# Kernel tuning notes

Measured on AMD Instinct MI355X. Metric: run time of the kernel, lower is better.

## Reference

```python
import jax, jax.numpy as jnp
import numpy as np

B, T, H, L, O = 128, 1024, 512, 2, 1
SCALE = 0.02  # keep tanh/sigmoid in sane range


def setup_inputs() -> dict:
    key = jax.random.key(0)
    ks = jax.random.split(key, 13)
    return {
        "input": jax.random.normal(ks[0], (B, 8), jnp.float32),
        "hidden": jax.random.normal(ks[1], (L, B, H), jnp.float32) * 0.5,
        "encoder_outputs": jax.random.normal(ks[2], (B, T, H), jnp.float32),
        "attn_w": jax.random.normal(ks[3], (1, (L + 1) * H), jnp.float32) * SCALE,
        "attn_b": jnp.zeros((1,), jnp.float32),
        "comb_w": jax.random.normal(ks[4], (H, H + O), jnp.float32) * SCALE,
        "comb_b": jnp.zeros((H,), jnp.float32),
        "gru_w_ih": jax.random.normal(ks[5], (L, 3 * H, H), jnp.float32) * SCALE,
        "gru_w_hh": jax.random.normal(ks[6], (L, 3 * H, H), jnp.float32) * SCALE,
        "gru_b_ih": jnp.zeros((L, 3 * H), jnp.float32),
        "gru_b_hh": jnp.zeros((L, 3 * H), jnp.float32),
        "out_w": jax.random.normal(ks[7], (O, H), jnp.float32) * SCALE,
        "out_b": jnp.zeros((O,), jnp.float32),
    }


def reference(input, hidden, encoder_outputs, attn_w, attn_b, comb_w, comb_b,
              gru_w_ih, gru_w_hh, gru_b_ih, gru_b_hh, out_w, out_b):
    # input0 = input[:, -1].unsqueeze(1) -> [B, 1]
    input0 = input[:, -1:]
    # hidden [L,B,H] -> hidden_attn [B, L*H]
    hidden_attn = jnp.transpose(hidden, (1, 0, 2)).reshape(hidden.shape[1], -1)
    # Vectorized additive-attention scores (original loops over T):
    # score[b,t] = [hidden_attn_b ; enc_bt] @ attn_w.T + attn_b
    w = attn_w[0]                      # [(L+1)*H]
    w_h, w_e = w[: L * H], w[L * H:]   # [L*H], [H]
    score = (hidden_attn @ w_h)[:, None] + jnp.einsum('bth,h->bt', encoder_outputs, w_e) + attn_b[0]
    attn_weights = jax.nn.softmax(score, axis=1)          # [B, T]
    attn_applied = jnp.einsum('bt,bth->bh', attn_weights, encoder_outputs)  # [B, H]
    # attn_combine + relu (dropout_p = 0 -> identity)
    comb_in = jnp.concatenate([input0, attn_applied], axis=1)  # [B, 1+H]
    x = jax.nn.relu(comb_in @ comb_w.T + comb_b)               # [B, H]
    # single-step multi-layer GRU (PyTorch gate order: r, z, n)
    new_hidden = []
    for l in range(L):
        gx = x @ gru_w_ih[l].T + gru_b_ih[l]             # [B, 3H]
        gh = hidden[l] @ gru_w_hh[l].T + gru_b_hh[l]     # [B, 3H]
        xr, xz, xn = jnp.split(gx, 3, axis=1)
        hr, hz, hn = jnp.split(gh, 3, axis=1)
        r = jax.nn.sigmoid(xr + hr)
        z = jax.nn.sigmoid(xz + hz)
        n = jnp.tanh(xn + r * hn)
        h_new = (1.0 - z) * n + z * hidden[l]
        new_hidden.append(h_new)
        x = h_new
    hidden_out = jnp.stack(new_hidden, axis=0)           # [L, B, H]
    output = x @ out_w.T + out_b                         # [B, O]
    return output, hidden_out, attn_weights[:, None, :]
```

## Files before the change

kernel.cpp:

```cpp
#include <hip/hip_runtime.h>
#include <math.h>

#define B 128
#define T 1024
#define H 512
#define L 2
#define G3H 1536
#define C 8
#define TC 128
#define TT 8
#define NT (TC / TT)
#define KS 4

#define GLOBAL_AS __attribute__((address_space(1)))
#define LDS_AS    __attribute__((address_space(3)))

__global__ __launch_bounds__(256, 4)
void attn_fused_kernel(const float* __restrict__ enc,
                       const float* __restrict__ attn_w,
                       float* __restrict__ score_out,
                       float* __restrict__ part,
                       float* __restrict__ stats) {
    int c = blockIdx.x, b = blockIdx.y;
    int tid = threadIdx.x, lane = tid & 63, wave = tid >> 6;
    __shared__ float tile[2][TT * H];
    __shared__ float s_tile[TT];

    const float4 we0 = *(const float4*)(attn_w + L * H + lane * 8);
    const float4 we1 = *(const float4*)(attn_w + L * H + lane * 8 + 4);

    const float* encb = enc + ((size_t)b * T + c * TC) * H;
    const GLOBAL_AS float* gsrc = (const GLOBAL_AS float*)encb;
    LDS_AS float* ldst = (LDS_AS float*)(&tile[0][0]);

#define STAGE(buf, t0)                                                        \
    {                                                                         \
        const GLOBAL_AS float* g = gsrc + (size_t)(t0) * H;                   \
        LDS_AS float* lb = ldst + (buf) * (TT * H);                           \
        _Pragma("unroll")                                                     \
        for (int k = 0; k < 4; k++) {                                         \
            __builtin_amdgcn_global_load_lds(                                 \
                (const GLOBAL_AS void*)(g + k * 1024 + tid * 4),              \
                (LDS_AS void*)(lb + k * 1024 + tid * 4), 16, 0, 0);           \
        }                                                                     \
    }

    float m_run = -1e30f, l_run = 0.0f;
    float accx = 0.0f, accy = 0.0f;

    STAGE(0, 0);
    for (int t = 0; t < NT; t++) {
        __syncthreads();
        if (t + 1 < NT) STAGE((t + 1) & 1, (t + 1) * TT);
        const float* tb = &tile[t & 1][0];

#pragma unroll
        for (int r = 0; r < 2; r++) {
            int row = wave * 2 + r;
            const float* tr = tb + row * H + lane * 8;
            float4 e0 = *(const float4*)(tr);
            float4 e1 = *(const float4*)(tr + 4);
            float d = e0.x * we0.x + e0.y * we0.y + e0.z * we0.z + e0.w * we0.w
                    + e1.x * we1.x + e1.y * we1.y + e1.z * we1.z + e1.w * we1.w;
#pragma unroll
            for (int off = 32; off; off >>= 1) d += __shfl_xor(d, off);
            if (lane == 0) {
                s_tile[row] = d;
                score_out[b * T + c * TC + t * TT + row] = d;
            }
        }
        __builtin_amdgcn_s_waitcnt(0xC07F);
        __builtin_amdgcn_s_barrier();

        float sarr[TT], tmax = -1e30f;
#pragma unroll
        for (int i = 0; i < TT; i++) {
            sarr[i] = s_tile[i];
            tmax = fmaxf(tmax, sarr[i]);
        }
        float m_new = fmaxf(m_run, tmax);
        float alpha = __expf(m_run - m_new);
        accx *= alpha; accy *= alpha;
        float wsum = 0.0f;
#pragma unroll
        for (int i = 0; i < TT; i++) {
            float w = __expf(sarr[i] - m_new);
            wsum += w;
            accx += w * tb[i * H + tid];
            accy += w * tb[i * H + tid + 256];
        }
        l_run = l_run * alpha + wsum;
        m_run = m_new;
    }
    part[((size_t)c * B + b) * H + tid]       = accx;
    part[((size_t)c * B + b) * H + tid + 256] = accy;
    if (tid == 0) {
        stats[(c * B + b) * 2]     = m_run;
        stats[(c * B + b) * 2 + 1] = l_run;
    }
#undef STAGE
}

__global__ void attn_reduce_kernel(const float* __restrict__ part,
                                   const float* __restrict__ stats,
                                   const float* __restrict__ score,
                                   float* __restrict__ attn_applied,
                                   float* __restrict__ attnw) {
    int b = blockIdx.x, tid = threadIdx.x;
    float mc[C], lc[C], m_fin = -1e30f;
#pragma unroll
    for (int k = 0; k < C; k++) {
        mc[k] = stats[(k * B + b) * 2];
        lc[k] = stats[(k * B + b) * 2 + 1];
        m_fin = fmaxf(m_fin, mc[k]);
    }
    float l_fin = 0.0f;
#pragma unroll
    for (int k = 0; k < C; k++) l_fin += lc[k] * __expf(mc[k] - m_fin);
    float inv = 1.0f / l_fin;
    float ax = 0.0f, ay = 0.0f;
#pragma unroll
    for (int k = 0; k < C; k++) {
        float sc = __expf(mc[k] - m_fin);
        ax += sc * part[((size_t)k * B + b) * H + tid];
        ay += sc * part[((size_t)k * B + b) * H + tid + 256];
    }
    attn_applied[(size_t)b * H + tid]       = ax * inv;
    attn_applied[(size_t)b * H + tid + 256] = ay * inv;
    float4 sv = *(const float4*)(score + b * T + tid * 4);
    float4 ov = { __expf(sv.x - m_fin) * inv, __expf(sv.y - m_fin) * inv,
                  __expf(sv.z - m_fin) * inv, __expf(sv.w - m_fin) * inv };
    *(float4*)(attnw + b * T + tid * 4) = ov;
}

__global__ void comb_kernel(const float* __restrict__ attn_applied,
                            const float* __restrict__ input,
                            const float* __restrict__ comb_w,
                            const float* __restrict__ comb_b,
                            float* __restrict__ x_out) {
    int q = blockIdx.x, b = blockIdx.y, tid = threadIdx.x;
    int lane = tid & 63, wave = tid >> 6;
    float in0 = input[b * 8 + 7];
    float areg[8];
#pragma unroll
    for (int j = 0; j < 8; j++) areg[j] = attn_applied[(size_t)b * H + j * 64 + lane];
    for (int r = 0; r < 32; r++) {
        int h = q * 128 + wave * 32 + r;
        const float* wr = comb_w + (size_t)h * (H + 1);
        float d = 0.0f;
#pragma unroll
        for (int j = 0; j < 8; j++) d += areg[j] * wr[1 + j * 64 + lane];
#pragma unroll
        for (int off = 32; off; off >>= 1) d += __shfl_xor(d, off);
        if (lane == 0)
            x_out[(size_t)b * H + h] = fmaxf(0.0f, d + in0 * wr[0] + comb_b[h]);
    }
}

__global__ void gemm_kernel(const float* __restrict__ A0,
                            const float* __restrict__ A1,
                            const float* __restrict__ W0,
                            const float* __restrict__ W1,
                            float* __restrict__ C0,
                            float* __restrict__ C1) {
    int z = blockIdx.z;
    int sel = z & 1, ks = z >> 1;
    const float* A = sel ? A1 : A0;
    const float* W = sel ? W1 : W0;
    float* Cp = (sel ? C1 : C0) + (size_t)ks * B * G3H;
    __shared__ float As[32][33];
    __shared__ float Ws[32][33];
    int n0 = blockIdx.x * 32, m0 = blockIdx.y * 32;
    int tid = threadIdx.x;
    int lrow = tid >> 3;
    int lcol = (tid & 7) * 4;
    int tm = (tid >> 4) * 2;
    int tn = (tid & 15) * 2;
    float a00 = 0, a01 = 0, a10 = 0, a11 = 0;
    int kbeg = ks * (H / KS), kend = kbeg + H / KS;
    for (int k0 = kbeg; k0 < kend; k0 += 32) {
        float4 av = *(const float4*)(A + (size_t)(m0 + lrow) * H + k0 + lcol);
        float4 wv = *(const float4*)(W + (size_t)(n0 + lrow) * H + k0 + lcol);
        __syncthreads();
        As[lrow][lcol] = av.x; As[lrow][lcol + 1] = av.y;
        As[lrow][lcol + 2] = av.z; As[lrow][lcol + 3] = av.w;
        Ws[lrow][lcol] = wv.x; Ws[lrow][lcol + 1] = wv.y;
        Ws[lrow][lcol + 2] = wv.z; Ws[lrow][lcol + 3] = wv.w;
        __syncthreads();
#pragma unroll
        for (int k = 0; k < 32; k++) {
            float x0 = As[tm][k], x1 = As[tm + 1][k];
            float w0 = Ws[tn][k], w1 = Ws[tn + 1][k];
            a00 += x0 * w0; a01 += x0 * w1;
            a10 += x1 * w0; a11 += x1 * w1;
        }
    }
    Cp[(size_t)(m0 + tm) * G3H + n0 + tn]         = a00;
    Cp[(size_t)(m0 + tm) * G3H + n0 + tn + 1]     = a01;
    Cp[(size_t)(m0 + tm + 1) * G3H + n0 + tn]     = a10;
    Cp[(size_t)(m0 + tm + 1) * G3H + n0 + tn + 1] = a11;
}

__global__ void gates_kernel(const float* __restrict__ gx,
                             const float* __restrict__ gh,
                             const float* __restrict__ b_ih,
                             const float* __restrict__ b_hh,
                             const float* __restrict__ hprev,
                             float* __restrict__ hid_out,
                             float* __restrict__ x_out) {
    int idx = blockIdx.x * 256 + threadIdx.x;
    int b = idx >> 9, h = idx & 511;
    size_t gb = (size_t)b * G3H;
    float xr = b_ih[h], xz = b_ih[H + h], xn = b_ih[2 * H + h];
    float hr = b_hh[h], hz = b_hh[H + h], hn = b_hh[2 * H + h];
#pragma unroll
    for (int k = 0; k < KS; k++) {
        size_t o = (size_t)k * B * G3H + gb;
        xr += gx[o + h];         xz += gx[o + H + h];     xn += gx[o + 2 * H + h];
        hr += gh[o + h];         hz += gh[o + H + h];     hn += gh[o + 2 * H + h];
    }
    float hp = hprev[(size_t)b * H + h];
    float r = 1.0f / (1.0f + expf(-(xr + hr)));
    float z = 1.0f / (1.0f + expf(-(xz + hz)));
    float n = tanhf(xn + r * hn);
    float hnew = (1.0f - z) * n + z * hp;
    hid_out[(size_t)b * H + h] = hnew;
    x_out[(size_t)b * H + h] = hnew;
}

__global__ void out_kernel(const float* __restrict__ x,
                           const float* __restrict__ out_w,
                           const float* __restrict__ out_b,
                           float* __restrict__ out) {
    int b = blockIdx.x, lane = threadIdx.x;
    const float4 w0 = *(const float4*)(out_w + lane * 8);
    const float4 w1 = *(const float4*)(out_w + lane * 8 + 4);
    const float4 x0 = *(const float4*)(x + (size_t)b * H + lane * 8);
    const float4 x1 = *(const float4*)(x + (size_t)b * H + lane * 8 + 4);
    float d = x0.x * w0.x + x0.y * w0.y + x0.z * w0.z + x0.w * w0.w
            + x1.x * w1.x + x1.y * w1.y + x1.z * w1.z + x1.w * w1.w;
#pragma unroll
    for (int off = 32; off; off >>= 1) d += __shfl_xor(d, off);
    if (lane == 0) out[b] = d + out_b[0];
}

extern "C" void kernel_launch(void* const* d_in, const int* in_sizes, int n_in,
                              void* d_out, int out_size, void* d_ws, size_t ws_size,
                              hipStream_t stream) {
    const float* input  = (const float*)d_in[0];
    const float* hidden = (const float*)d_in[1];
    const float* enc    = (const float*)d_in[2];
    const float* attn_w = (const float*)d_in[3];
    const float* comb_w = (const float*)d_in[5];
    const float* comb_b = (const float*)d_in[6];
    const float* w_ih   = (const float*)d_in[7];
    const float* w_hh   = (const float*)d_in[8];
    const float* b_ih   = (const float*)d_in[9];
    const float* b_hh   = (const float*)d_in[10];
    const float* out_w  = (const float*)d_in[11];
    const float* out_b  = (const float*)d_in[12];

    float* out = (float*)d_out;
    float* hid_out = out + B;
    float* attnw   = out + B + L * B * H;

    float* ws      = (float*)d_ws;
    float* score   = ws;
    float* part    = score + B * T;
    float* stats   = part + C * B * H;
    float* attnapp = stats + C * B * 2;
    float* x       = attnapp + B * H;
    float* gx      = x + B * H;
    float* gh      = gx + KS * B * G3H;

    attn_fused_kernel<<<dim3(C, B), 256, 0, stream>>>(enc, attn_w, score, part, stats);
    attn_reduce_kernel<<<dim3(B), 256, 0, stream>>>(part, stats, score, attnapp, attnw);
    comb_kernel<<<dim3(4, B), 256, 0, stream>>>(attnapp, input, comb_w, comb_b, x);

    for (int l = 0; l < L; l++) {
        const float* hl = hidden + (size_t)l * B * H;
        gemm_kernel<<<dim3(G3H / 32, B / 32, 2 * KS), 256, 0, stream>>>(
            x, hl,
            w_ih + (size_t)l * G3H * H, w_hh + (size_t)l * G3H * H,
            gx, gh);
        gates_kernel<<<dim3(B * H / 256), 256, 0, stream>>>(
            gx, gh, b_ih + l * G3H, b_hh + l * G3H, hl,
            hid_out + (size_t)l * B * H, x);
    }
    out_kernel<<<dim3(B), 64, 0, stream>>>(x, out_w, out_b, out);
}
```

Baseline: 459.5 us.

## Replace fp32 tiled GRU GEMM with bf16 MFMA matrix-core kernel

The shared-memory fp32 GEMM for the GRU gate projections is replaced by a single-wavefront kernel that converts fp32 operands to bf16 in registers and issues 16x16x32 bf16 MFMA instructions, computing a 64x16 output tile per wave. The K-split factor is also halved, which reduces the partial-sum traffic the gates kernel has to read back. The intent is to move this matmul onto the matrix cores and drop the LDS staging and barriers. In exchange, operands are rounded to bf16, which lowers precision, and each 64-thread block loads its fragments straight from global memory with no reuse through LDS.

Result: faster. 445.4 us (-3.1%).

```diff
diff --git a/kernel.cpp b/kernel.cpp
--- a/kernel.cpp
+++ b/kernel.cpp
@@ -10,10 +10,13 @@
 #define TC 128
 #define TT 8
 #define NT (TC / TT)
-#define KS 4
+#define KS 2
 
 #define GLOBAL_AS __attribute__((address_space(1)))
 #define LDS_AS    __attribute__((address_space(3)))
+
+typedef __attribute__((ext_vector_type(8))) short bf16x8;
+typedef __attribute__((ext_vector_type(4))) float f32x4;
 
 __global__ __launch_bounds__(256, 4)
 void attn_fused_kernel(const float* __restrict__ enc,
@@ -157,48 +160,61 @@
     }
 }
 
-__global__ void gemm_kernel(const float* __restrict__ A0,
-                            const float* __restrict__ A1,
-                            const float* __restrict__ W0,
-                            const float* __restrict__ W1,
-                            float* __restrict__ C0,
-                            float* __restrict__ C1) {
-    int z = blockIdx.z;
-    int sel = z & 1, ks = z >> 1;
+__device__ inline short f2bf(float f) {
+    union { float f; unsigned u; } v; v.f = f;
+    unsigned r = v.u + 0x7fffu + ((v.u >> 16) & 1u);
+    return (short)(r >> 16);
+}
+
+__device__ inline bf16x8 load_frag(const float* __restrict__ p) {
+    float4 a = *(const float4*)p;
+    float4 b = *(const float4*)(p + 4);
+    bf16x8 r;
+    r[0] = f2bf(a.x); r[1] = f2bf(a.y); r[2] = f2bf(a.z); r[3] = f2bf(a.w);
+    r[4] = f2bf(b.x); r[5] = f2bf(b.y); r[6] = f2bf(b.z); r[7] = f2bf(b.w);
+    return r;
+}
+
+__global__ __launch_bounds__(64)
+void gemm_mfma_kernel(const float* __restrict__ A0,
+                      const float* __restrict__ A1,
+                      const float* __restrict__ W0,
+                      const float* __restrict__ W1,
+                      float* __restrict__ C0,
+                      float* __restrict__ C1) {
+    int job = blockIdx.x;
+    int sel = job & 1, ks = (job >> 1) & (KS - 1), mh = (job >> 2) & 1, nt = job >> 3;
     const float* A = sel ? A1 : A0;
     const float* W = sel ? W1 : W0;
     float* Cp = (sel ? C1 : C0) + (size_t)ks * B * G3H;
-    __shared__ float As[32][33];
-    __shared__ float Ws[32][33];
-    int n0 = blockIdx.x * 32, m0 = blockIdx.y * 32;
-    int tid = threadIdx.x;
-    int lrow = tid >> 3;
-    int lcol = (tid & 7) * 4;
-    int tm = (tid >> 4) * 2;
-    int tn = (tid & 15) * 2;
-    float a00 = 0, a01 = 0, a10 = 0, a11 = 0;
-    int kbeg = ks * (H / KS), kend = kbeg + H / KS;
-    for (int k0 = kbeg; k0 < kend; k0 += 32) {
-        float4 av = *(const float4*)(A + (size_t)(m0 + lrow) * H + k0 + lcol);
-        float4 wv = *(const float4*)(W + (size_t)(n0 + lrow) * H + k0 + lcol);
-        __syncthreads();
-        As[lrow][lcol] = av.x; As[lrow][lcol + 1] = av.y;
-        As[lrow][lcol + 2] = av.z; As[lrow][lcol + 3] = av.w;
-        Ws[lrow][lcol] = wv.x; Ws[lrow][lcol + 1] = wv.y;
-        Ws[lrow][lcol + 2] = wv.z; Ws[lrow][lcol + 3] = wv.w;
-        __syncthreads();
-#pragma unroll
-        for (int k = 0; k < 32; k++) {
-            float x0 = As[tm][k], x1 = As[tm + 1][k];
-            float w0 = Ws[tn][k], w1 = Ws[tn + 1][k];
-            a00 += x0 * w0; a01 += x0 * w1;
-            a10 += x1 * w0; a11 += x1 * w1;
-        }
-    }
-    Cp[(size_t)(m0 + tm) * G3H + n0 + tn]         = a00;
-    Cp[(size_t)(m0 + tm) * G3H + n0 + tn + 1]     = a01;
-    Cp[(size_t)(m0 + tm + 1) * G3H + n0 + tn]     = a10;
-    Cp[(size_t)(m0 + tm + 1) * G3H + n0 + tn + 1] = a11;
+    int lane = threadIdx.x;
+    int row16 = lane & 15, quad = lane >> 4;
+    int n0 = nt * 16, m0 = mh * 64;
+    int kb = ks * (H / KS);
+    const float* Wp = W + (size_t)(n0 + row16) * H + kb + quad * 8;
+    const float* Ap = A + (size_t)(m0 + row16) * H + kb + quad * 8;
+    f32x4 acc0 = {0.f, 0.f, 0.f, 0.f}, acc1 = acc0, acc2 = acc0, acc3 = acc0;
+#pragma unroll 2
+    for (int k = 0; k < H / KS; k += 32) {
+        bf16x8 bw = load_frag(Wp + k);
+        bf16x8 a0 = load_frag(Ap + k);
+        bf16x8 a1 = load_frag(Ap + 16 * H + k);
+        bf16x8 a2 = load_frag(Ap + 32 * H + k);
+        bf16x8 a3 = load_frag(Ap + 48 * H + k);
+        acc0 = __builtin_amdgcn_mfma_f32_16x16x32_bf16(a0, bw, acc0, 0, 0, 0);
+        acc1 = __builtin_amdgcn_mfma_f32_16x16x32_bf16(a1, bw, acc1, 0, 0, 0);
+        acc2 = __builtin_amdgcn_mfma_f32_16x16x32_bf16(a2, bw, acc2, 0, 0, 0);
+        acc3 = __builtin_amdgcn_mfma_f32_16x16x32_bf16(a3, bw, acc3, 0, 0, 0);
+    }
+    int col = n0 + row16;
+    int rb = m0 + quad * 4;
+#pragma unroll
+    for (int reg = 0; reg < 4; reg++) {
+        Cp[(size_t)(rb + reg) * G3H + col]      = acc0[reg];
+        Cp[(size_t)(rb + 16 + reg) * G3H + col] = acc1[reg];
+        Cp[(size_t)(rb + 32 + reg) * G3H + col] = acc2[reg];
+        Cp[(size_t)(rb + 48 + reg) * G3H + col] = acc3[reg];
+    }
 }
 
 __global__ void gates_kernel(const float* __restrict__ gx,
@@ -279,7 +295,7 @@
 
     for (int l = 0; l < L; l++) {
         const float* hl = hidden + (size_t)l * B * H;
-        gemm_kernel<<<dim3(G3H / 32, B / 32, 2 * KS), 256, 0, stream>>>(
+        gemm_mfma_kernel<<<dim3((G3H / 16) * 2 * KS * 2), 64, 0, stream>>>(
             x, hl,
             w_ih + (size_t)l * G3H * H, w_hh + (size_t)l * G3H * H,
             gx, gh);
```
